# Kernel optimization log

Measured on AMD Instinct MI355X. Metric: run time of the kernel, lower is better.

Reference implementation:

```python
import jax, jax.numpy as jnp
import numpy as np

N = 8192
D = 384


def setup_inputs() -> dict:
    key = jax.random.key(0)
    kx, kq, kk, kv, kf = jax.random.split(key, 5)
    x = jax.random.normal(kx, (N, D), dtype=jnp.float32)
    Wq = jax.random.uniform(kq, (D, D), dtype=jnp.float32)
    Wk = jax.random.uniform(kk, (D, D), dtype=jnp.float32)
    Wv = jax.random.uniform(kv, (D, D), dtype=jnp.float32)
    ffws = jax.random.uniform(kf, (D,), dtype=jnp.float32)
    return {"x": x, "Wq": Wq, "Wk": Wk, "Wv": Wv, "ffws": ffws}


def reference(x, Wq, Wk, Wv, ffws):
    def layer(h):
        # Q = Wq @ h.T -> Q.T = h @ Wq.T ; scores = Q.T @ K = (h Wq.T)(Wk h.T)
        Qt = h @ Wq.T                    # [N, D]
        K = Wk @ h.T                     # [D, N]
        scores = jax.nn.softmax(Qt @ K, axis=1)  # [N, N], torch implicit dim=1
        Vt = h @ Wv.T                    # [N, D]
        # weighted_sum double-loop == scores @ Vt (soft_sim is square so
        # choice(size()) always returns N)
        return scores @ Vt               # [N, D]

    z = layer(layer(x))
    # o = sigmoid(sum(ffws * z[-1]))
    return jax.nn.sigmoid(jnp.sum(ffws * z[-1]))
```

## Files before the change

kernel.cpp:

```cpp
#include <hip/hip_runtime.h>
#include <hip/hip_bf16.h>
#include <math.h>

static constexpr int kN = 8192;
static constexpr int kD = 384;
static constexpr int kND = kN * kD;

typedef __attribute__((ext_vector_type(8))) short short8;
typedef __attribute__((ext_vector_type(4))) float f32x4;

__device__ __forceinline__ ushort f2bf(float f) {
  union { float f; unsigned int i; } cv; cv.f = f;
  unsigned int lsb = (cv.i >> 16) & 1u;
  unsigned int r = cv.i + 0x7fffu + lsb;
  return (ushort)(r >> 16);
}
__device__ __forceinline__ float bf2f(ushort u) {
  union { unsigned int i; float f; } cv; cv.i = ((unsigned int)u) << 16;
  return cv.f;
}
__device__ __forceinline__ f32x4 mfma_bf16(short8 a, short8 b, f32x4 c) {
  return __builtin_amdgcn_mfma_f32_16x16x32_bf16(a, b, c, 0, 0, 0);
}
__device__ __forceinline__ void bar_lds() {
  asm volatile("s_waitcnt lgkmcnt(0)" ::: "memory");
  __builtin_amdgcn_s_barrier();
}

__global__ __launch_bounds__(512) void proj_mfma(
    const float* __restrict__ x, const float* __restrict__ Wq,
    const float* __restrict__ Wk, const float* __restrict__ Wv,
    ushort* __restrict__ Qh, ushort* __restrict__ Kh,
    ushort* __restrict__ VTh)
{
  __shared__ ushort XH[128 * 32], XL[128 * 32];
  __shared__ ushort WH[3][96 * 32], WL[3][96 * 32];

  const int tid = threadIdx.x;
  const int w = tid >> 6;
  const int lane = tid & 63;
  const int l15 = lane & 15;
  const int hi4 = lane >> 4;
  const int i0 = blockIdx.x * 128;
  const int j0 = blockIdx.y * 96;
  const float* Wm[3] = {Wq, Wk, Wv};

  const f32x4 zf = {0.f, 0.f, 0.f, 0.f};
  f32x4 acc[3][6];
#pragma unroll
  for (int m = 0; m < 3; ++m)
#pragma unroll
    for (int ct = 0; ct < 6; ++ct) acc[m][ct] = zf;

  const int xrow = tid >> 2;
  const int xc8 = (tid & 3) * 8;

  for (int dc = 0; dc < 12; ++dc) {
    const int d0 = dc * 32;
    {
      const float* src = x + (size_t)(i0 + xrow) * kD + d0 + xc8;
      const float4 v0 = *reinterpret_cast<const float4*>(src);
      const float4 v1 = *reinterpret_cast<const float4*>(src + 4);
      const float vs[8] = {v0.x, v0.y, v0.z, v0.w, v1.x, v1.y, v1.z, v1.w};
      ushort hh[8], ll[8];
#pragma unroll
      for (int j = 0; j < 8; ++j) {
        const ushort h = f2bf(vs[j]);
        hh[j] = h;
        ll[j] = f2bf(vs[j] - bf2f(h));
      }
      *reinterpret_cast<uint4*>(&XH[xrow * 32 + xc8]) =
          *reinterpret_cast<const uint4*>(hh);
      *reinterpret_cast<uint4*>(&XL[xrow * 32 + xc8]) =
          *reinterpret_cast<const uint4*>(ll);
    }
    if (tid < 384) {
#pragma unroll
      for (int m = 0; m < 3; ++m) {
        const float* src = Wm[m] + (size_t)(j0 + xrow) * kD + d0 + xc8;
        const float4 v0 = *reinterpret_cast<const float4*>(src);
        const float4 v1 = *reinterpret_cast<const float4*>(src + 4);
        const float vs[8] = {v0.x, v0.y, v0.z, v0.w, v1.x, v1.y, v1.z, v1.w};
        ushort hh[8], ll[8];
#pragma unroll
        for (int j = 0; j < 8; ++j) {
          const ushort h = f2bf(vs[j]);
          hh[j] = h;
          ll[j] = f2bf(vs[j] - bf2f(h));
        }
        *reinterpret_cast<uint4*>(&WH[m][xrow * 32 + xc8]) =
            *reinterpret_cast<const uint4*>(hh);
        *reinterpret_cast<uint4*>(&WL[m][xrow * 32 + xc8]) =
            *reinterpret_cast<const uint4*>(ll);
      }
    }
    __syncthreads();
    const short8 xa = *reinterpret_cast<const short8*>(
        &XH[(16 * w + l15) * 32 + 8 * hi4]);
    const short8 xb = *reinterpret_cast<const short8*>(
        &XL[(16 * w + l15) * 32 + 8 * hi4]);
#pragma unroll
    for (int m = 0; m < 3; ++m) {
#pragma unroll
      for (int ct = 0; ct < 6; ++ct) {
        const short8 wh = *reinterpret_cast<const short8*>(
            &WH[m][(16 * ct + l15) * 32 + 8 * hi4]);
        const short8 wl = *reinterpret_cast<const short8*>(
            &WL[m][(16 * ct + l15) * 32 + 8 * hi4]);
        acc[m][ct] = mfma_bf16(xa, wh, acc[m][ct]);
        acc[m][ct] = mfma_bf16(xa, wl, acc[m][ct]);
        acc[m][ct] = mfma_bf16(xb, wh, acc[m][ct]);
      }
    }
    __syncthreads();
  }

#pragma unroll
  for (int ct = 0; ct < 6; ++ct)
#pragma unroll
    for (int r = 0; r < 4; ++r) {
      const size_t oi =
          (size_t)(i0 + 16 * w + 4 * hi4 + r) * kD + j0 + 16 * ct + l15;
      Qh[oi] = f2bf(acc[0][ct][r]);
      Kh[oi] = f2bf(acc[1][ct][r]);
    }
#pragma unroll
  for (int ct = 0; ct < 6; ++ct) {
    ushort4 h;
    ushort* hp = &h.x;
#pragma unroll
    for (int r = 0; r < 4; ++r) hp[r] = f2bf(acc[2][ct][r]);
    *reinterpret_cast<ushort4*>(
        &VTh[(size_t)(j0 + 16 * ct + l15) * kN + i0 + 16 * w + 4 * hi4]) = h;
  }
}

static constexpr int SPLITf = 4;
static constexpr int KEYSf = kN / SPLITf;
static constexpr int NTIL = KEYSf / 128;

static constexpr int OFF_QH = 0;
static constexpr int OFF_P  = 50176;

__global__ __launch_bounds__(512, 2) void flash_mfma(
    const ushort* __restrict__ Qh,
    const ushort* __restrict__ Kh,
    const ushort* __restrict__ VTh,
    ushort* __restrict__ Opart, float* __restrict__ ml)
{
  __shared__ ushort LDSU[67584];
  __shared__ float MLB[2048];

  const int tid = threadIdx.x;
  const int w = tid >> 6;
  const int lane = tid & 63;
  const int l15 = lane & 15;
  const int hi4 = lane >> 4;
  const int sp = blockIdx.x;
  const int i0 = blockIdx.y * 128;
  const int kg0 = sp * KEYSf;

  {
    const int row = tid >> 2;
    const int sg = (tid & 3) * 96;
    const ushort* sh = Qh + (size_t)(i0 + row) * kD + sg;
    ushort* dh = LDSU + OFF_QH + row * 392 + sg;
#pragma unroll
    for (int u = 0; u < 12; ++u)
      *reinterpret_cast<uint4*>(dh + 8 * u) =
          *reinterpret_cast<const uint4*>(sh + 8 * u);
  }

  const f32x4 zf = {0.f, 0.f, 0.f, 0.f};
  f32x4 o[8][3];
#pragma unroll
  for (int qt = 0; qt < 8; ++qt)
#pragma unroll
    for (int c = 0; c < 3; ++c) o[qt][c] = zf;
  float m_run[8], l_run[8];
#pragma unroll
  for (int qt = 0; qt < 8; ++qt) { m_run[qt] = -INFINITY; l_run[qt] = 0.f; }

  __syncthreads();

  for (int kb = 0; kb < NTIL; ++kb) {
    const int kg = kg0 + kb * 128;

    f32x4 sacc[8];
#pragma unroll
    for (int qt = 0; qt < 8; ++qt) sacc[qt] = zf;
    const size_t kbase = (size_t)(kg + 16 * w + l15) * kD + 8 * hi4;
    short8 ka[12];
#pragma unroll
    for (int ks = 0; ks < 12; ++ks)
      ka[ks] = *reinterpret_cast<const short8*>(Kh + kbase + 32 * ks);
    __builtin_amdgcn_sched_barrier(0);
#pragma unroll
    for (int ks = 0; ks < 12; ++ks) {
      const int d0 = 32 * ks;
#pragma unroll
      for (int qt = 0; qt < 8; ++qt) {
        const short8 qh = *reinterpret_cast<const short8*>(
            LDSU + OFF_QH + (16 * qt + l15) * 392 + d0 + 8 * hi4);
        sacc[qt] = mfma_bf16(ka[ks], qh, sacc[qt]);
      }
    }

#pragma unroll
    for (int qt = 0; qt < 8; ++qt) {
      float mt = fmaxf(fmaxf(sacc[qt][0], sacc[qt][1]),
                       fmaxf(sacc[qt][2], sacc[qt][3]));
      mt = fmaxf(mt, __shfl_xor(mt, 16, 64));
      mt = fmaxf(mt, __shfl_xor(mt, 32, 64));
      if (lane < 16) MLB[(qt * 16 + l15) * 8 + w] = mt;
    }
    bar_lds();

    short8 vv[12];
#pragma unroll
    for (int c = 0; c < 3; ++c)
#pragma unroll
      for (int kv = 0; kv < 4; ++kv)
        vv[c * 4 + kv] = *reinterpret_cast<const short8*>(
            VTh + (size_t)(48 * w + 16 * c + l15) * kN + kg + 32 * kv + 8 * hi4);
    __builtin_amdgcn_sched_barrier(0);

    float sc[8];
#pragma unroll
    for (int qt = 0; qt < 8; ++qt) {
      const float4 ma =
          *reinterpret_cast<const float4*>(&MLB[(qt * 16 + l15) * 8]);
      const float4 mb =
          *reinterpret_cast<const float4*>(&MLB[(qt * 16 + l15) * 8 + 4]);
      const float Mt = fmaxf(fmaxf(fmaxf(ma.x, ma.y), fmaxf(ma.z, ma.w)),
                             fmaxf(fmaxf(mb.x, mb.y), fmaxf(mb.z, mb.w)));
      const float mnew = fmaxf(m_run[qt], Mt);
      sc[qt] = __expf(m_run[qt] - mnew);
      m_run[qt] = mnew;
      const float p0 = __expf(sacc[qt][0] - mnew);
      const float p1 = __expf(sacc[qt][1] - mnew);
      const float p2 = __expf(sacc[qt][2] - mnew);
      const float p3 = __expf(sacc[qt][3] - mnew);
      float ls = (p0 + p1) + (p2 + p3);
      ls += __shfl_xor(ls, 16, 64);
      ls += __shfl_xor(ls, 32, 64);
      if (lane < 16) MLB[1024 + (qt * 16 + l15) * 8 + w] = ls;
      uint2 HH;
      HH.x = (unsigned int)f2bf(p0) | ((unsigned int)f2bf(p1) << 16);
      HH.y = (unsigned int)f2bf(p2) | ((unsigned int)f2bf(p3) << 16);
      const int pi = (16 * qt + l15) * 136 + 16 * w + 4 * hi4;
      *reinterpret_cast<uint2*>(LDSU + OFF_P + pi) = HH;
#pragma unroll
      for (int r = 0; r < 4; ++r) {
        const float scr_ = __shfl(sc[qt], 4 * hi4 + r, 64);
#pragma unroll
        for (int c = 0; c < 3; ++c) o[qt][c][r] *= scr_;
      }
    }
    bar_lds();
#pragma unroll
    for (int qt = 0; qt < 8; ++qt) {
      const float4 la =
          *reinterpret_cast<const float4*>(&MLB[1024 + (qt * 16 + l15) * 8]);
      const float4 lb =
          *reinterpret_cast<const float4*>(&MLB[1024 + (qt * 16 + l15) * 8 + 4]);
      const float ls = ((la.x + la.y) + (la.z + la.w)) +
                       ((lb.x + lb.y) + (lb.z + lb.w));
      l_run[qt] = l_run[qt] * sc[qt] + ls;
    }

#pragma unroll
    for (int kv = 0; kv < 4; ++kv) {
      short8 pf[8];
#pragma unroll
      for (int qt = 0; qt < 8; ++qt)
        pf[qt] = *reinterpret_cast<const short8*>(
            LDSU + OFF_P + (16 * qt + l15) * 136 + 32 * kv + 8 * hi4);
#pragma unroll
      for (int c = 0; c < 3; ++c) {
#pragma unroll
        for (int qt = 0; qt < 8; ++qt)
          o[qt][c] = mfma_bf16(pf[qt], vv[c * 4 + kv], o[qt][c]);
      }
    }
  }

#pragma unroll
  for (int qt = 0; qt < 8; ++qt) {
    const float linv = 1.0f / l_run[qt];
#pragma unroll
    for (int r = 0; r < 4; ++r) {
      const float lr = __shfl(linv, 4 * hi4 + r, 64);
#pragma unroll
      for (int c = 0; c < 3; ++c)
        Opart[(size_t)sp * kND + (i0 + 16 * qt + 4 * hi4 + r) * kD +
              48 * w + 16 * c + l15] = f2bf(o[qt][c][r] * lr);
    }
  }
  if (w == 0 && lane < 16) {
#pragma unroll
    for (int qt = 0; qt < 8; ++qt) {
      const int mi = (sp * kN + i0 + 16 * qt + l15) * 2;
      ml[mi] = m_run[qt];
      ml[mi + 1] = l_run[qt];
    }
  }
}

__global__ __launch_bounds__(256) void merge_kernel(
    const ushort* __restrict__ Opart, const float* __restrict__ ml,
    float* __restrict__ O)
{
  const size_t idx = (size_t)blockIdx.x * 256 + threadIdx.x;
  const size_t i = idx / kD;
  float m = ml[i * 2];
#pragma unroll
  for (int sp = 1; sp < SPLITf; ++sp)
    m = fmaxf(m, ml[((size_t)sp * kN + i) * 2]);
  float den = 0.f, acc = 0.f;
#pragma unroll
  for (int sp = 0; sp < SPLITf; ++sp) {
    const float e = __expf(ml[((size_t)sp * kN + i) * 2] - m) *
                    ml[((size_t)sp * kN + i) * 2 + 1];
    den += e;
    acc += e * bf2f(Opart[(size_t)sp * kND + idx]);
  }
  O[idx] = acc / den;
}

__global__ __launch_bounds__(64) void qrow_kernel(
    const float* __restrict__ h1, const float* __restrict__ Wq,
    float* __restrict__ q2)
{
  const int j = blockIdx.x;
  const int lane = threadIdx.x;
  const float* hr = h1 + (size_t)(kN - 1) * kD;
  float acc = 0.f;
  for (int d = lane; d < kD; d += 64) acc += hr[d] * Wq[(size_t)j * kD + d];
#pragma unroll
  for (int off = 32; off > 0; off >>= 1) acc += __shfl_xor(acc, off, 64);
  if (lane == 0) q2[j] = acc;
}

__global__ __launch_bounds__(384) void u_kernel(
    const float* __restrict__ Wk, const float* __restrict__ q2,
    float* __restrict__ u)
{
  __shared__ float qs[kD];
  const int d = threadIdx.x;
  qs[d] = q2[d];
  __syncthreads();
  float acc = 0.f;
  for (int k = 0; k < kD; ++k) acc += Wk[(size_t)k * kD + d] * qs[k];
  u[d] = acc;
}

__global__ __launch_bounds__(256) void logits_kernel(
    const float* __restrict__ h1, const float* __restrict__ u,
    float* __restrict__ lg)
{
  const int wave = threadIdx.x >> 6;
  const int lane = threadIdx.x & 63;
  const int j = blockIdx.x * 4 + wave;
  float acc = 0.f;
#pragma unroll
  for (int t = 0; t < kD / 64; ++t) {
    const int d = lane + t * 64;
    acc += h1[(size_t)j * kD + d] * u[d];
  }
#pragma unroll
  for (int off = 32; off > 0; off >>= 1) acc += __shfl_xor(acc, off, 64);
  if (lane == 0) lg[j] = acc;
}

__global__ __launch_bounds__(1024) void smax_kernel(
    const float* __restrict__ lg, float* __restrict__ wgt)
{
  __shared__ float red[16];
  const int t = threadIdx.x;
  const int wave = t >> 6;
  const int lane = t & 63;
  float v[8];
  float mx = -INFINITY;
#pragma unroll
  for (int s = 0; s < 8; ++s) {
    v[s] = lg[t + 1024 * s];
    mx = fmaxf(mx, v[s]);
  }
#pragma unroll
  for (int off = 32; off > 0; off >>= 1) mx = fmaxf(mx, __shfl_xor(mx, off, 64));
  if (lane == 0) red[wave] = mx;
  __syncthreads();
  if (t == 0) {
    float m = red[0];
    for (int i = 1; i < 16; ++i) m = fmaxf(m, red[i]);
    red[0] = m;
  }
  __syncthreads();
  const float m = red[0];
  __syncthreads();
  float sum = 0.f;
#pragma unroll
  for (int s = 0; s < 8; ++s) {
    v[s] = expf(v[s] - m);
    sum += v[s];
  }
#pragma unroll
  for (int off = 32; off > 0; off >>= 1) sum += __shfl_xor(sum, off, 64);
  if (lane == 0) red[wave] = sum;
  __syncthreads();
  if (t == 0) {
    float S = 0.f;
    for (int i = 0; i < 16; ++i) S += red[i];
    red[0] = S;
  }
  __syncthreads();
  const float invS = 1.0f / red[0];
#pragma unroll
  for (int s = 0; s < 8; ++s) wgt[t + 1024 * s] = v[s] * invS;
}

__global__ __launch_bounds__(384) void wsum_kernel(
    const float* __restrict__ wgt, const float* __restrict__ h1,
    float* __restrict__ part)
{
  __shared__ float wl[256];
  const int b = blockIdx.x;
  const int t = threadIdx.x;
  if (t < 256) wl[t] = wgt[b * 256 + t];
  __syncthreads();
  const float* Hp = h1 + (size_t)b * 256 * kD;
  float acc = 0.f;
  for (int j = 0; j < 256; ++j) acc += wl[j] * Hp[(size_t)j * kD + t];
  part[b * kD + t] = acc;
}

__global__ __launch_bounds__(384) void final2_kernel(
    const float* __restrict__ part, const float* __restrict__ Wv,
    const float* __restrict__ ffws, float* __restrict__ out)
{
  __shared__ float zs[kD];
  __shared__ float red[6];
  const int t = threadIdx.x;
  const int wave = t >> 6;
  const int lane = t & 63;
  float z = 0.f;
#pragma unroll
  for (int b = 0; b < 32; ++b) z += part[b * kD + t];
  zs[t] = z;
  __syncthreads();
  float zv = 0.f;
  for (int k = 0; k < kD; ++k) zv += Wv[(size_t)t * kD + k] * zs[k];
  float val = zv * ffws[t];
#pragma unroll
  for (int off = 32; off > 0; off >>= 1) val += __shfl_xor(val, off, 64);
  if (lane == 0) red[wave] = val;
  __syncthreads();
  if (t == 0) {
    float s = red[0];
    for (int i = 1; i < 6; ++i) s += red[i];
    out[0] = 1.0f / (1.0f + expf(-s));
  }
}

extern "C" void kernel_launch(void* const* d_in, const int* in_sizes, int n_in,
                              void* d_out, int out_size, void* d_ws, size_t ws_size,
                              hipStream_t stream) {
  const float* x    = (const float*)d_in[0];
  const float* Wq   = (const float*)d_in[1];
  const float* Wk   = (const float*)d_in[2];
  const float* Wv   = (const float*)d_in[3];
  const float* ffws = (const float*)d_in[4];
  float* out = (float*)d_out;
  char* wsb = (char*)d_ws;

  ushort* Qh  = (ushort*)wsb;
  ushort* Kh  = Qh + kND;
  ushort* VTh = Kh + kND;
  ushort* Opart = VTh + kND;
  float* ml    = (float*)(Opart + (size_t)SPLITf * kND);
  float* h1    = ml + (size_t)SPLITf * kN * 2;
  float* q2    = h1 + (size_t)kND;
  float* u     = q2 + kD;
  float* lg    = u + kD;
  float* wgt   = lg + kN;
  float* part  = wgt + kN;

  proj_mfma<<<dim3(kN / 128, kD / 96), 512, 0, stream>>>(
      x, Wq, Wk, Wv, Qh, Kh, VTh);
  flash_mfma<<<dim3(SPLITf, kN / 128), 512, 0, stream>>>(
      Qh, Kh, VTh, Opart, ml);
  merge_kernel<<<(kN * kD) / 256, 256, 0, stream>>>(Opart, ml, h1);
  qrow_kernel<<<kD, 64, 0, stream>>>(h1, Wq, q2);
  u_kernel<<<1, 384, 0, stream>>>(Wk, q2, u);
  logits_kernel<<<kN / 4, 256, 0, stream>>>(h1, u, lg);
  smax_kernel<<<1, 1024, 0, stream>>>(lg, wgt);
  wsum_kernel<<<32, 384, 0, stream>>>(wgt, h1, part);
  final2_kernel<<<1, 384, 0, stream>>>(part, Wv, ffws, out);
}
```

Measured before the change: 284.8 us.

## Double-buffer K tiles in registers and fuse qrow/u kernels

The flash attention loop now prefetches the next tile's K fragments into a second register buffer right after the QK MFMAs. It alternates the two buffers across an unrolled-by-two loop, so global K loads overlap the softmax and PV work. Separately, the qrow and u kernels are merged into one single-block kernel that keeps q2 in shared memory, removing a launch and a global round trip. The risks are higher register pressure from the extra buffer, a prefetch past the last tile that reads into adjacent workspace memory, and a serialized single-block q computation.

```diff
diff --git a/kernel.cpp b/kernel.cpp
--- a/kernel.cpp
+++ b/kernel.cpp
@@ -181,20 +181,22 @@
 #pragma unroll
   for (int qt = 0; qt < 8; ++qt) { m_run[qt] = -INFINITY; l_run[qt] = 0.f; }
 
-  __syncthreads();
-
-  for (int kb = 0; kb < NTIL; ++kb) {
+  short8 kA[12], kB[12];
+  {
+    const size_t kb0 = (size_t)(kg0 + 16 * w + l15) * kD + 8 * hi4;
+#pragma unroll
+    for (int ks = 0; ks < 12; ++ks)
+      kA[ks] = *reinterpret_cast<const short8*>(Kh + kb0 + 32 * ks);
+  }
+
+  __syncthreads();
+
+  auto tile_body = [&](int kb, short8 (&KC)[12], short8 (&KN)[12]) {
     const int kg = kg0 + kb * 128;
 
     f32x4 sacc[8];
 #pragma unroll
     for (int qt = 0; qt < 8; ++qt) sacc[qt] = zf;
-    const size_t kbase = (size_t)(kg + 16 * w + l15) * kD + 8 * hi4;
-    short8 ka[12];
-#pragma unroll
-    for (int ks = 0; ks < 12; ++ks)
-      ka[ks] = *reinterpret_cast<const short8*>(Kh + kbase + 32 * ks);
-    __builtin_amdgcn_sched_barrier(0);
 #pragma unroll
     for (int ks = 0; ks < 12; ++ks) {
       const int d0 = 32 * ks;
@@ -202,9 +204,18 @@
       for (int qt = 0; qt < 8; ++qt) {
         const short8 qh = *reinterpret_cast<const short8*>(
             LDSU + OFF_QH + (16 * qt + l15) * 392 + d0 + 8 * hi4);
-        sacc[qt] = mfma_bf16(ka[ks], qh, sacc[qt]);
+        sacc[qt] = mfma_bf16(KC[ks], qh, sacc[qt]);
       }
     }
+    __builtin_amdgcn_sched_barrier(0);
+
+    {
+      const size_t kbn = (size_t)(kg + 128 + 16 * w + l15) * kD + 8 * hi4;
+#pragma unroll
+      for (int ks = 0; ks < 12; ++ks)
+        KN[ks] = *reinterpret_cast<const short8*>(Kh + kbn + 32 * ks);
+    }
+    __builtin_amdgcn_sched_barrier(0);
 
 #pragma unroll
     for (int qt = 0; qt < 8; ++qt) {
@@ -283,6 +294,11 @@
           o[qt][c] = mfma_bf16(pf[qt], vv[c * 4 + kv], o[qt][c]);
       }
     }
+  };
+
+  for (int kb2 = 0; kb2 < NTIL; kb2 += 2) {
+    tile_body(kb2, kA, kB);
+    tile_body(kb2 + 1, kB, kA);
   }
 
 #pragma unroll
@@ -328,31 +344,31 @@
   O[idx] = acc / den;
 }
 
-__global__ __launch_bounds__(64) void qrow_kernel(
+__global__ __launch_bounds__(384) void qu_kernel(
     const float* __restrict__ h1, const float* __restrict__ Wq,
-    float* __restrict__ q2)
-{
-  const int j = blockIdx.x;
-  const int lane = threadIdx.x;
+    const float* __restrict__ Wk, float* __restrict__ u)
+{
+  __shared__ float q2s[kD];
+  const int t = threadIdx.x;
+  const int wv = t >> 6;
+  const int lane = t & 63;
   const float* hr = h1 + (size_t)(kN - 1) * kD;
-  float acc = 0.f;
-  for (int d = lane; d < kD; d += 64) acc += hr[d] * Wq[(size_t)j * kD + d];
-#pragma unroll
-  for (int off = 32; off > 0; off >>= 1) acc += __shfl_xor(acc, off, 64);
-  if (lane == 0) q2[j] = acc;
-}
-
-__global__ __launch_bounds__(384) void u_kernel(
-    const float* __restrict__ Wk, const float* __restrict__ q2,
-    float* __restrict__ u)
-{
-  __shared__ float qs[kD];
-  const int d = threadIdx.x;
-  qs[d] = q2[d];
-  __syncthreads();
-  float acc = 0.f;
-  for (int k = 0; k < kD; ++k) acc += Wk[(size_t)k * kD + d] * qs[k];
-  u[d] = acc;
+  for (int jj = 0; jj < 64; ++jj) {
+    const int j = wv * 64 + jj;
+    float acc = 0.f;
+#pragma unroll
+    for (int tt = 0; tt < kD / 64; ++tt) {
+      const int d = lane + tt * 64;
+      acc += hr[d] * Wq[(size_t)j * kD + d];
+    }
+#pragma unroll
+    for (int off = 32; off > 0; off >>= 1) acc += __shfl_xor(acc, off, 64);
+    if (lane == 0) q2s[j] = acc;
+  }
+  __syncthreads();
+  float au = 0.f;
+  for (int k = 0; k < kD; ++k) au += Wk[(size_t)k * kD + t] * q2s[k];
+  u[t] = au;
 }
 
 __global__ __launch_bounds__(256) void logits_kernel(
@@ -480,8 +496,7 @@
   ushort* Opart = VTh + kND;
   float* ml    = (float*)(Opart + (size_t)SPLITf * kND);
   float* h1    = ml + (size_t)SPLITf * kN * 2;
-  float* q2    = h1 + (size_t)kND;
-  float* u     = q2 + kD;
+  float* u     = h1 + (size_t)kND;
   float* lg    = u + kD;
   float* wgt   = lg + kN;
   float* part  = wgt + kN;
@@ -491,8 +506,7 @@
   flash_mfma<<<dim3(SPLITf, kN / 128), 512, 0, stream>>>(
       Qh, Kh, VTh, Opart, ml);
   merge_kernel<<<(kN * kD) / 256, 256, 0, stream>>>(Opart, ml, h1);
-  qrow_kernel<<<kD, 64, 0, stream>>>(h1, Wq, q2);
-  u_kernel<<<1, 384, 0, stream>>>(Wk, q2, u);
+  qu_kernel<<<1, 384, 0, stream>>>(h1, Wq, Wk, u);
   logits_kernel<<<kN / 4, 256, 0, stream>>>(h1, u, lg);
   smax_kernel<<<1, 1024, 0, stream>>>(lg, wgt);
   wsum_kernel<<<32, 384, 0, stream>>>(wgt, h1, part);
```

Measured after the change: 568.0 us. +99.5%, slower.
